# Optimization experiments

Hardware: AMD Instinct MI355X
Metric: run time of the kernel (lower is better)

## Reference

```python
import jax, jax.numpy as jnp
import numpy as np

B, D, T = 8, 512, 2048
K = 8192


def setup_inputs() -> dict:
    key = jax.random.key(0)
    k1, k2 = jax.random.split(key)
    latents = jax.random.normal(k1, (B, D, T), dtype=jnp.float32)
    # nn.Embedding weight init: uniform(-1/K, 1/K)
    embedding = jax.random.uniform(k2, (K, D), dtype=jnp.float32,
                                   minval=-1.0 / K, maxval=1.0 / K)
    return {"latents": latents, "embedding": embedding}


def reference(latents, embedding):
    # latents: [B, D, T] -> [B, T, D]
    x = jnp.transpose(latents, (0, 2, 1))
    # squared Euclidean distances (argmin identical to cdist p=2 argmin)
    x2 = jnp.sum(x * x, axis=-1, keepdims=True)          # [B, T, 1]
    e2 = jnp.sum(embedding * embedding, axis=-1)          # [K]
    xe = jnp.einsum('btd,kd->btk', x, embedding)          # [B, T, K]
    d2 = x2 - 2.0 * xe + e2                               # [B, T, K]
    ids = jnp.argmin(d2, axis=-1)                         # [B, T] int
    quantized = embedding[ids]                            # [B, T, D] gather
    return jnp.transpose(quantized, (0, 2, 1))            # [B, D, T]
```

## Files before the change

### kernel.cpp

```cpp
#include <hip/hip_runtime.h>

#define B 8
#define D 512
#define T 2048
#define K 8192
#define M (B*T)

typedef float f32x4 __attribute__((ext_vector_type(4)));
typedef short bf16x8 __attribute__((ext_vector_type(8)));
typedef unsigned short us8 __attribute__((ext_vector_type(8)));

#define CAP_SEG 48
#define WIN 1.6e-3f

#define WS_X2    0
#define WS_E2    65536
#define WS_CNT   98304
#define WS_IDS   163840
#define WS_OVFC  229376
#define WS_OVFL  229632
#define WS_BEST  295168
#define WS_GMIN  426240
#define WS_LIST  491776
#define WS_AX    6783232
#define WS_BE    23560448
#define WS_NEED  31949056

__device__ inline unsigned short f2bf(float f) {
    unsigned int x = __float_as_uint(f);
    unsigned int r = x + 0x7fffu + ((x >> 16) & 1u);
    return (unsigned short)(r >> 16);
}

__device__ inline unsigned int f2ord(float f) {
    unsigned int u = __float_as_uint(f);
    return (u & 0x80000000u) ? ~u : (u | 0x80000000u);
}
__device__ inline float ord2f(unsigned int u) {
    return __uint_as_float((u & 0x80000000u) ? (u & 0x7fffffffu) : ~u);
}

__device__ inline void gload16(const void* g, void* l) {
    __builtin_amdgcn_global_load_lds(
        (const __attribute__((address_space(1))) unsigned int*)g,
        (__attribute__((address_space(3))) unsigned int*)l, 16, 0, 0);
}

__global__ __launch_bounds__(256)
void vq_x2_init(const float* __restrict__ lat, float* __restrict__ x2g,
                unsigned int* __restrict__ cnt_seg_u32, int* __restrict__ ovfc,
                unsigned int* __restrict__ gmin) {
#pragma clang fp contract(off)
    int p = blockIdx.x * 256 + threadIdx.x;
    cnt_seg_u32[p] = 0;
    gmin[p] = 0xFFFFFFFFu;
    if (p == 0) *ovfc = 0;
    int b = p / T, t = p % T;
    const float* base = lat + (size_t)b * D * T + t;
    float blk[4];
#pragma unroll
    for (int q = 0; q < 4; q++) {
        float r[8];
#pragma unroll
        for (int j = 0; j < 8; j++) {
            float v = base[(size_t)(q * 128 + j) * T];
            r[j] = __fmul_rn(v, v);
        }
        for (int i = 8; i < 128; i += 8) {
#pragma unroll
            for (int j = 0; j < 8; j++) {
                float v = base[(size_t)(q * 128 + i + j) * T];
                r[j] = __fadd_rn(r[j], __fmul_rn(v, v));
            }
        }
        blk[q] = __fadd_rn(__fadd_rn(__fadd_rn(r[0], r[1]), __fadd_rn(r[2], r[3])),
                           __fadd_rn(__fadd_rn(r[4], r[5]), __fadd_rn(r[6], r[7])));
    }
    x2g[p] = __fadd_rn(__fadd_rn(blk[0], blk[1]), __fadd_rn(blk[2], blk[3]));
}

__global__ __launch_bounds__(256)
void vq_x2_kernel(const float* __restrict__ lat, float* __restrict__ x2g) {
#pragma clang fp contract(off)
    int p = blockIdx.x * 256 + threadIdx.x;
    int b = p / T, t = p % T;
    const float* base = lat + (size_t)b * D * T + t;
    float blk[4];
#pragma unroll
    for (int q = 0; q < 4; q++) {
        float r[8];
#pragma unroll
        for (int j = 0; j < 8; j++) {
            float v = base[(size_t)(q * 128 + j) * T];
            r[j] = __fmul_rn(v, v);
        }
        for (int i = 8; i < 128; i += 8) {
#pragma unroll
            for (int j = 0; j < 8; j++) {
                float v = base[(size_t)(q * 128 + i + j) * T];
                r[j] = __fadd_rn(r[j], __fmul_rn(v, v));
            }
        }
        blk[q] = __fadd_rn(__fadd_rn(__fadd_rn(r[0], r[1]), __fadd_rn(r[2], r[3])),
                           __fadd_rn(__fadd_rn(r[4], r[5]), __fadd_rn(r[6], r[7])));
    }
    x2g[p] = __fadd_rn(__fadd_rn(blk[0], blk[1]), __fadd_rn(blk[2], blk[3]));
}

__global__ __launch_bounds__(256)
void vq_e2_kernel(const float* __restrict__ emb, float* __restrict__ e2g) {
#pragma clang fp contract(off)
    int k = blockIdx.x * 256 + threadIdx.x;
    const float* base = emb + (size_t)k * D;
    float blk[4];
#pragma unroll
    for (int q = 0; q < 4; q++) {
        float r[8];
        {
            float4 a = *(const float4*)&base[q * 128];
            float4 c = *(const float4*)&base[q * 128 + 4];
            r[0] = __fmul_rn(a.x, a.x); r[1] = __fmul_rn(a.y, a.y);
            r[2] = __fmul_rn(a.z, a.z); r[3] = __fmul_rn(a.w, a.w);
            r[4] = __fmul_rn(c.x, c.x); r[5] = __fmul_rn(c.y, c.y);
            r[6] = __fmul_rn(c.z, c.z); r[7] = __fmul_rn(c.w, c.w);
        }
        for (int i = 8; i < 128; i += 8) {
            float4 a = *(const float4*)&base[q * 128 + i];
            float4 c = *(const float4*)&base[q * 128 + i + 4];
            r[0] = __fadd_rn(r[0], __fmul_rn(a.x, a.x));
            r[1] = __fadd_rn(r[1], __fmul_rn(a.y, a.y));
            r[2] = __fadd_rn(r[2], __fmul_rn(a.z, a.z));
            r[3] = __fadd_rn(r[3], __fmul_rn(a.w, a.w));
            r[4] = __fadd_rn(r[4], __fmul_rn(c.x, c.x));
            r[5] = __fadd_rn(r[5], __fmul_rn(c.y, c.y));
            r[6] = __fadd_rn(r[6], __fmul_rn(c.z, c.z));
            r[7] = __fadd_rn(r[7], __fmul_rn(c.w, c.w));
        }
        blk[q] = __fadd_rn(__fadd_rn(__fadd_rn(r[0], r[1]), __fadd_rn(r[2], r[3])),
                           __fadd_rn(__fadd_rn(r[4], r[5]), __fadd_rn(r[6], r[7])));
    }
    e2g[k] = __fadd_rn(__fadd_rn(blk[0], blk[1]), __fadd_rn(blk[2], blk[3]));
}

__global__ __launch_bounds__(256)
void vq_prep_a(const float* __restrict__ lat, unsigned short* __restrict__ Ax) {
    __shared__ float xsl[64][65];
    const int tid = threadIdx.x;
    const int m0 = blockIdx.x * 64;
    const int b = m0 / T, t0 = m0 % T;
    const float* lp = lat + (size_t)b * D * T + t0;
    for (int d0 = 0; d0 < D; d0 += 64) {
        if (d0) __syncthreads();
#pragma unroll
        for (int i = 0; i < 16; i++) {
            int idx = tid + i * 256;
            int dd = idx >> 6, tt = idx & 63;
            xsl[dd][tt] = lp[(size_t)(d0 + dd) * T + tt];
        }
        __syncthreads();
        int tt = tid & 63, g = tid >> 6;
        us8 va, vb;
#pragma unroll
        for (int j = 0; j < 8; j++) va[j] = f2bf(xsl[g * 16 + j][tt]);
#pragma unroll
        for (int j = 0; j < 8; j++) vb[j] = f2bf(xsl[g * 16 + 8 + j][tt]);
        *(us8*)&Ax[(size_t)(m0 + tt) * 512 + d0 + g * 16] = va;
        *(us8*)&Ax[(size_t)(m0 + tt) * 512 + d0 + g * 16 + 8] = vb;
    }
}

__global__ __launch_bounds__(256)
void vq_prep_b(const float* __restrict__ emb, unsigned short* __restrict__ Be) {
    size_t i = ((size_t)blockIdx.x * 256 + threadIdx.x) * 4;
    float4 v = *(const float4*)&emb[i];
    ushort4 o;
    o.x = f2bf(v.x); o.y = f2bf(v.y); o.z = f2bf(v.z); o.w = f2bf(v.w);
    *(ushort4*)&Be[i] = o;
}

#define BMg 128
#define BNg 128
#define NCHUNK 2048
#define NSTEPS ((NCHUNK / BNg) * 8)

__global__ __launch_bounds__(256, 2)
void vq_gemm(const unsigned short* __restrict__ Ax,
             const unsigned short* __restrict__ Be,
             const float* __restrict__ e2g,
             unsigned int* __restrict__ gmin,
             unsigned char* __restrict__ cnt_seg,
             unsigned short* __restrict__ list) {
    __shared__ unsigned short As[2][BMg * 64];
    __shared__ unsigned short Bs[2][BNg * 64];
    __shared__ float e2s[NCHUNK];
    __shared__ int cntl[BMg];

    const int tid = threadIdx.x;
    const int lane = tid & 63;
    const int wid = tid >> 6;
    const int m0 = blockIdx.x * BMg;
    const int nc0 = blockIdx.y * NCHUNK;

    for (int i = tid; i < NCHUNK; i += 256) e2s[i] = e2g[nc0 + i];
    if (tid < BMg) cntl[tid] = 0;
    asm volatile("s_waitcnt lgkmcnt(0)" ::: "memory");

    const int rbase = wid * 8 + (lane >> 3);
    const int cbyte = (((lane & 7) ^ (lane >> 3)) * 16);
    const char* gA = (const char*)Ax + (size_t)(m0 + rbase) * 1024 + cbyte;
    const char* gB = (const char*)Be + (size_t)(nc0 + rbase) * 1024 + cbyte;
    const int ldsoff = wid * 1024;

    const int rbyteA = (wid * 32 + (lane & 15)) * 128;
    const int rbyteB = ((lane & 15)) * 128;

#pragma unroll
    for (int i = 0; i < 4; i++) {
        gload16(gA + (size_t)i * 32768, (char*)As[0] + ldsoff + i * 4096);
        gload16(gB + (size_t)i * 32768, (char*)Bs[0] + ldsoff + i * 4096);
    }

    float runmin[2][4];
    float thrg[2][4];
#pragma unroll
    for (int mi = 0; mi < 2; mi++)
#pragma unroll
        for (int r = 0; r < 4; r++) runmin[mi][r] = 3.4e38f;

    f32x4 acc[2][8];
    for (int s = 0; s < NSTEPS; s++) {
        const int cur = s & 1;
        const int nt = s >> 3, ks = s & 7;

        __builtin_amdgcn_s_barrier();

        if (s + 1 < NSTEPS) {
            const int nt2 = (s + 1) >> 3, ks2 = (s + 1) & 7;
            const char* ga = gA + (size_t)(ks2 * 128);
            const char* gb = gB + (size_t)(nt2 * 128) * 1024 + (size_t)(ks2 * 128);
            char* la = (char*)As[cur ^ 1] + ldsoff;
            char* lb = (char*)Bs[cur ^ 1] + ldsoff;
#pragma unroll
            for (int i = 0; i < 4; i++) {
                gload16(ga + (size_t)i * 32768, la + i * 4096);
                gload16(gb + (size_t)i * 32768, lb + i * 4096);
            }
            asm volatile("s_waitcnt vmcnt(8)" ::: "memory");
        } else {
            asm volatile("s_waitcnt vmcnt(0)" ::: "memory");
        }
        __builtin_amdgcn_s_barrier();

        if (ks == 0) {
#pragma unroll
            for (int mi = 0; mi < 2; mi++)
#pragma unroll
                for (int ni = 0; ni < 8; ni++) acc[mi][ni] = (f32x4){0.f, 0.f, 0.f, 0.f};
#pragma unroll
            for (int mi = 0; mi < 2; mi++)
#pragma unroll
                for (int r = 0; r < 4; r++) {
                    const int m = m0 + wid * 32 + mi * 16 + (lane >> 4) * 4 + r;
                    thrg[mi][r] = ord2f(gmin[m]);
                }
        }

        __builtin_amdgcn_s_setprio(1);
#pragma unroll
        for (int kh = 0; kh < 2; kh++) {
            const int cb = ((((lane >> 4) + kh * 4) ^ (lane & 7)) * 16);
            bf16x8 af[2], bfr[8];
#pragma unroll
            for (int mi = 0; mi < 2; mi++)
                af[mi] = *(const bf16x8*)((const char*)As[cur] + rbyteA + mi * 2048 + cb);
#pragma unroll
            for (int ni = 0; ni < 8; ni++)
                bfr[ni] = *(const bf16x8*)((const char*)Bs[cur] + rbyteB + ni * 2048 + cb);
#pragma unroll
            for (int mi = 0; mi < 2; mi++)
#pragma unroll
                for (int ni = 0; ni < 8; ni++)
                    acc[mi][ni] = __builtin_amdgcn_mfma_f32_16x16x32_bf16(
                        af[mi], bfr[ni], acc[mi][ni], 0, 0, 0);
        }
        __builtin_amdgcn_s_setprio(0);

        if (ks == 7) {
            const int n0l = nt * BNg;
#pragma unroll
            for (int mi = 0; mi < 2; mi++)
#pragma unroll
                for (int ni = 0; ni < 8; ni++) {
                    float e2v = e2s[n0l + ni * 16 + (lane & 15)];
#pragma unroll
                    for (int r = 0; r < 4; r++)
                        acc[mi][ni][r] = e2v - 2.0f * acc[mi][ni][r];
                }
#pragma unroll
            for (int mi = 0; mi < 2; mi++)
#pragma unroll
                for (int r = 0; r < 4; r++) {
                    float v = acc[mi][0][r];
#pragma unroll
                    for (int ni = 1; ni < 8; ni++) v = fminf(v, acc[mi][ni][r]);
                    v = fminf(v, __shfl_xor(v, 1));
                    v = fminf(v, __shfl_xor(v, 2));
                    v = fminf(v, __shfl_xor(v, 4));
                    v = fminf(v, __shfl_xor(v, 8));
                    runmin[mi][r] = fminf(runmin[mi][r], v);
                    const int rloc = wid * 32 + mi * 16 + (lane >> 4) * 4 + r;
                    const int m = m0 + rloc;
                    float th = fminf(thrg[mi][r], runmin[mi][r]) + WIN;
#pragma unroll
                    for (int ni = 0; ni < 8; ni++) {
                        if (acc[mi][ni][r] < th) {
                            int kcode = nc0 + n0l + ni * 16 + (lane & 15);
                            int slot = atomicAdd(&cntl[rloc], 1);
                            if (slot < CAP_SEG)
                                list[m * 192 + blockIdx.y * CAP_SEG + slot] =
                                    (unsigned short)kcode;
                        }
                    }
                    if ((lane & 15) == 0)
                        atomicMin(&gmin[m], f2ord(runmin[mi][r]));
                }
        }
    }

    __syncthreads();
    if (tid < BMg) {
        int c = cntl[tid];
        cnt_seg[(size_t)(m0 + tid) * 4 + blockIdx.y] =
            (unsigned char)(c > 255 ? 255 : c);
    }
}

__global__ __launch_bounds__(256)
void vq_rescore3(const float* __restrict__ lat, const float* __restrict__ emb,
                 const float* __restrict__ x2g, const float* __restrict__ e2g,
                 const unsigned char* __restrict__ cnt_seg,
                 const unsigned short* __restrict__ list,
                 int* __restrict__ ids, int* __restrict__ ovfc,
                 int* __restrict__ ovfl, unsigned long long* __restrict__ best,
                 float* __restrict__ out) {
#pragma clang fp contract(off)
    __shared__ float xs[D][32];
    __shared__ unsigned long long bests[8][32];
    __shared__ int kid_s[32];

    const int tid = threadIdx.x;
    const int w = tid >> 5;
    const int l = tid & 31;
    const int m0 = blockIdx.x * 32;
    const int b = m0 / T, t0 = m0 % T;
    const int p = m0 + l;
    const size_t lbase = (size_t)b * D * T + t0;

#pragma unroll
    for (int i = 0; i < 64; i++) {
        int idx = tid + i * 256;
        int dd = idx >> 5, tt = idx & 31;
        xs[dd][tt] = lat[lbase + (size_t)dd * T + tt];
    }

    unsigned int cs = *(const unsigned int*)&cnt_seg[(size_t)p * 4];
    int c0 = cs & 255, c1 = (cs >> 8) & 255, c2 = (cs >> 16) & 255, c3 = (cs >> 24) & 255;
    const bool ovf = (c0 > CAP_SEG) | (c1 > CAP_SEG) | (c2 > CAP_SEG) | (c3 > CAP_SEG);
    if (w == 0 && ovf) {
        int s = atomicAdd(ovfc, 1);
        ovfl[s] = p;
        best[p] = ~0ull;
    }
    __syncthreads();

    const float x2v = x2g[p];
    unsigned long long bb = ~0ull;
    if (!ovf) {
        int segc[4] = {c0, c1, c2, c3};
#pragma unroll
        for (int seg = 0; seg < 4; seg++) {
            for (int j = w; j < segc[seg]; j += 8) {
                int k = list[(size_t)p * 192 + seg * CAP_SEG + j];
                const float4* er4 = (const float4*)(emb + (size_t)k * D);
                float acc = 0.f;
#pragma unroll 4
                for (int q = 0; q < D / 4; q++) {
                    float4 e4 = er4[q];
                    acc = __fadd_rn(acc, __fmul_rn(xs[q * 4 + 0][l], e4.x));
                    acc = __fadd_rn(acc, __fmul_rn(xs[q * 4 + 1][l], e4.y));
                    acc = __fadd_rn(acc, __fmul_rn(xs[q * 4 + 2][l], e4.z));
                    acc = __fadd_rn(acc, __fmul_rn(xs[q * 4 + 3][l], e4.w));
                }
                float tmp = __fsub_rn(x2v, __fadd_rn(acc, acc));
                float dist = __fadd_rn(tmp, e2g[k]);
                unsigned long long pk = ((unsigned long long)f2ord(dist) << 32) |
                                        (unsigned long long)(unsigned int)k;
                bb = (pk < bb) ? pk : bb;
            }
        }
    }
    bests[w][l] = bb;
    __syncthreads();

    if (tid < 32) {
        unsigned int cs2 = *(const unsigned int*)&cnt_seg[(size_t)(m0 + tid) * 4];
        bool ov2 = ((cs2 & 255) > CAP_SEG) | (((cs2 >> 8) & 255) > CAP_SEG) |
                   (((cs2 >> 16) & 255) > CAP_SEG) | (((cs2 >> 24) & 255) > CAP_SEG);
        if (!ov2) {
            unsigned long long v = bests[0][tid];
#pragma unroll
            for (int i = 1; i < 8; i++) v = (bests[i][tid] < v) ? bests[i][tid] : v;
            int kk = (int)(v & 0xFFFFFFFFull);
            ids[m0 + tid] = kk;
            kid_s[tid] = kk;
        } else {
            kid_s[tid] = -1;
        }
    }
    __syncthreads();

    float* ebuf = &xs[0][0];
    float* outb = out + (size_t)b * D * T + t0;
    for (int d0 = 0; d0 < D; d0 += 64) {
        if (d0) __syncthreads();
#pragma unroll
        for (int i = 0; i < 8; i++) {
            int idx = tid + i * 256;
            int tt = idx >> 6, dd = idx & 63;
            int kk = kid_s[tt];
            ebuf[tt * 65 + dd] = emb[(size_t)(kk < 0 ? 0 : kk) * D + d0 + dd];
        }
        __syncthreads();
#pragma unroll
        for (int i = 0; i < 8; i++) {
            int idx = tid + i * 256;
            int tt = idx & 31, dd = idx >> 5;
            if (kid_s[tt] >= 0)
                outb[(size_t)(d0 + dd) * T + tt] = ebuf[tt * 65 + dd];
        }
    }
}

__global__ __launch_bounds__(256)
void vq_fallback_par(const float* __restrict__ lat, const float* __restrict__ emb,
                     const float* __restrict__ x2g, const float* __restrict__ e2g,
                     const int* __restrict__ ovfc, const int* __restrict__ ovfl,
                     unsigned long long* __restrict__ best) {
#pragma clang fp contract(off)
    __shared__ float xr[D];
    __shared__ unsigned long long wmin[4];
    const int n = *ovfc;
    const int ntask = n * 8;
    for (int task = blockIdx.x; task < ntask; task += gridDim.x) {
        const int m = ovfl[task >> 3];
        const int slice = task & 7;
        const int b = m / T, t = m % T;
        for (int d = threadIdx.x; d < D; d += 256)
            xr[d] = lat[(size_t)b * D * T + (size_t)d * T + t];
        __syncthreads();
        const float x2v = x2g[m];
        unsigned long long bl = ~0ull;
        for (int k = slice * 1024 + threadIdx.x; k < slice * 1024 + 1024; k += 256) {
            const float* er = emb + (size_t)k * D;
            float s = 0.f;
            for (int d = 0; d < D; d++)
                s = __fadd_rn(s, __fmul_rn(xr[d], er[d]));
            float tmp = __fsub_rn(x2v, __fadd_rn(s, s));
            float dist = __fadd_rn(tmp, e2g[k]);
            unsigned long long pk = ((unsigned long long)f2ord(dist) << 32) |
                                    (unsigned long long)(unsigned int)k;
            bl = (pk < bl) ? pk : bl;
        }
#pragma unroll
        for (int off = 1; off < 64; off <<= 1) {
            unsigned long long o = __shfl_xor(bl, off);
            bl = (o < bl) ? o : bl;
        }
        if ((threadIdx.x & 63) == 0) wmin[threadIdx.x >> 6] = bl;
        __syncthreads();
        if (threadIdx.x == 0) {
            unsigned long long v = wmin[0];
            for (int i = 1; i < 4; i++) v = (wmin[i] < v) ? wmin[i] : v;
            atomicMin(&best[m], v);
        }
        __syncthreads();
    }
}

__global__ __launch_bounds__(256)
void vq_finalize(const int* __restrict__ ovfc, const int* __restrict__ ovfl,
                 const unsigned long long* __restrict__ best, int* __restrict__ ids) {
    const int n = *ovfc;
    for (int i = blockIdx.x * 256 + threadIdx.x; i < n; i += gridDim.x * 256) {
        int m = ovfl[i];
        ids[m] = (int)(best[m] & 0xFFFFFFFFull);
    }
}

__global__ __launch_bounds__(256)
void vq_gather_ovf(const float* __restrict__ emb, const int* __restrict__ ovfc,
                   const int* __restrict__ ovfl, const int* __restrict__ ids,
                   float* __restrict__ out) {
    const int n = *ovfc;
    for (int i = blockIdx.x; i < n; i += gridDim.x) {
        int m = ovfl[i];
        int b = m / T, t = m % T;
        int k = ids[m];
        for (int d = threadIdx.x; d < D; d += 256)
            out[(size_t)b * D * T + (size_t)d * T + t] = emb[(size_t)k * D + d];
    }
}

#define TM 64
#define TN 128
#define TD 32
__global__ __launch_bounds__(256)
void vq_main_old(const float* __restrict__ latents, const float* __restrict__ emb,
                 const float* __restrict__ x2g, const float* __restrict__ e2g,
                 float* __restrict__ out) {
#pragma clang fp contract(off)
    __shared__ __align__(16) float xs[TD][TM];
    __shared__ __align__(16) float es[TD][TN + 4];
    __shared__ float e2s[TN];
    __shared__ float x2s[TM];
    __shared__ int ids_s[TM];
    __shared__ __align__(16) float gbuf[64][65];
    const int tid = threadIdx.x;
    const int tn = tid & 15;
    const int tm = tid >> 4;
    const int m0 = blockIdx.x * TM;
    const int b = m0 / T;
    const int t0 = m0 % T;
    const float* lat = latents + (size_t)b * D * T + t0;
    if (tid < TM) x2s[tid] = x2g[m0 + tid];
    float minv[4];
    int mini[4];
#pragma unroll
    for (int i = 0; i < 4; i++) { minv[i] = 3.4e38f; mini[i] = 0; }
    for (int k0 = 0; k0 < K; k0 += TN) {
        __syncthreads();
        if (tid < TN) e2s[tid] = e2g[k0 + tid];
        float s[4][8];
#pragma unroll
        for (int i = 0; i < 4; i++)
#pragma unroll
            for (int j = 0; j < 8; j++) s[i][j] = 0.0f;
        for (int d0 = 0; d0 < D; d0 += TD) {
            if (d0) __syncthreads();
#pragma unroll
            for (int i = 0; i < 8; i++) {
                int idx = tid + i * 256;
                int dd = idx >> 6, tt = idx & 63;
                xs[dd][tt] = lat[(size_t)(d0 + dd) * T + tt];
            }
#pragma unroll
            for (int i = 0; i < 16; i++) {
                int idx = tid + i * 256;
                int nn = idx >> 5, dd = idx & 31;
                es[dd][nn] = emb[(size_t)(k0 + nn) * D + d0 + dd];
            }
            __syncthreads();
#pragma unroll
            for (int d = 0; d < TD; d++) {
                float4 xr = *(const float4*)&xs[d][tm * 4];
                float4 ea = *(const float4*)&es[d][tn * 4];
                float4 eb = *(const float4*)&es[d][64 + tn * 4];
                float xv[4] = {xr.x, xr.y, xr.z, xr.w};
                float ev[8] = {ea.x, ea.y, ea.z, ea.w, eb.x, eb.y, eb.z, eb.w};
#pragma unroll
                for (int i = 0; i < 4; i++)
#pragma unroll
                    for (int j = 0; j < 8; j++)
                        s[i][j] = __fadd_rn(s[i][j], __fmul_rn(xv[i], ev[j]));
            }
        }
#pragma unroll
        for (int i = 0; i < 4; i++) {
            float x2v = x2s[tm * 4 + i];
#pragma unroll
            for (int j = 0; j < 8; j++) {
                int col = (j < 4) ? (tn * 4 + j) : (64 + tn * 4 + (j - 4));
                float s2 = __fadd_rn(s[i][j], s[i][j]);
                float tmp = __fsub_rn(x2v, s2);
                float dist = __fadd_rn(tmp, e2s[col]);
                int kk = k0 + col;
                if (dist < minv[i]) { minv[i] = dist; mini[i] = kk; }
            }
        }
    }
#pragma unroll
    for (int i = 0; i < 4; i++) {
        float v1 = minv[i];
        int i1 = mini[i];
#pragma unroll
        for (int off = 1; off < 16; off <<= 1) {
            float ov = __shfl_xor(v1, off);
            int oi = __shfl_xor(i1, off);
            if (ov < v1 || (ov == v1 && oi < i1)) { v1 = ov; i1 = oi; }
        }
        if (tn == 0) ids_s[tm * 4 + i] = i1;
    }
    __syncthreads();
    float* outb = out + (size_t)b * D * T + t0;
    for (int d0 = 0; d0 < D; d0 += 64) {
        if (d0) __syncthreads();
#pragma unroll
        for (int i = 0; i < 16; i++) {
            int idx = tid + i * 256;
            int tt = idx >> 6, dd = idx & 63;
            gbuf[tt][dd] = emb[(size_t)ids_s[tt] * D + d0 + dd];
        }
        __syncthreads();
#pragma unroll
        for (int i = 0; i < 16; i++) {
            int idx = tid + i * 256;
            int dd = idx >> 6, tt = idx & 63;
            outb[(size_t)(d0 + dd) * T + tt] = gbuf[tt][dd];
        }
    }
}

extern "C" void kernel_launch(void* const* d_in, const int* in_sizes, int n_in,
                              void* d_out, int out_size, void* d_ws, size_t ws_size,
                              hipStream_t stream) {
    const float* latents = (const float*)d_in[0];
    const float* emb     = (const float*)d_in[1];
    float* out = (float*)d_out;
    char* ws = (char*)d_ws;
    float* x2g = (float*)(ws + WS_X2);
    float* e2g = (float*)(ws + WS_E2);

    if (ws_size < (size_t)WS_NEED) {
        hipLaunchKernelGGL(vq_x2_kernel, dim3(M / 256), dim3(256), 0, stream, latents, x2g);
        hipLaunchKernelGGL(vq_e2_kernel, dim3(K / 256), dim3(256), 0, stream, emb, e2g);
        hipLaunchKernelGGL(vq_main_old, dim3(M / TM), dim3(256), 0, stream,
                           latents, emb, x2g, e2g, out);
        return;
    }

    unsigned char* cnt_seg = (unsigned char*)(ws + WS_CNT);
    int* ids = (int*)(ws + WS_IDS);
    int* ovfc = (int*)(ws + WS_OVFC);
    int* ovfl = (int*)(ws + WS_OVFL);
    unsigned long long* best = (unsigned long long*)(ws + WS_BEST);
    unsigned int* gmin = (unsigned int*)(ws + WS_GMIN);
    unsigned short* list = (unsigned short*)(ws + WS_LIST);
    unsigned short* Ax = (unsigned short*)(ws + WS_AX);
    unsigned short* Be = (unsigned short*)(ws + WS_BE);

    hipLaunchKernelGGL(vq_x2_init, dim3(M / 256), dim3(256), 0, stream,
                       latents, x2g, (unsigned int*)cnt_seg, ovfc, gmin);
    hipLaunchKernelGGL(vq_e2_kernel, dim3(K / 256), dim3(256), 0, stream, emb, e2g);
    hipLaunchKernelGGL(vq_prep_a, dim3(M / 64), dim3(256), 0, stream, latents, Ax);
    hipLaunchKernelGGL(vq_prep_b, dim3((K * D) / 1024), dim3(256), 0, stream, emb, Be);
    hipLaunchKernelGGL(vq_gemm, dim3(M / BMg, K / NCHUNK), dim3(256), 0, stream,
                       Ax, Be, e2g, gmin, cnt_seg, list);
    hipLaunchKernelGGL(vq_rescore3, dim3(M / 32), dim3(256), 0, stream,
                       latents, emb, x2g, e2g, cnt_seg, list, ids, ovfc, ovfl, best, out);
    hipLaunchKernelGGL(vq_fallback_par, dim3(512), dim3(256), 0, stream,
                       latents, emb, x2g, e2g, ovfc, ovfl, best);
    hipLaunchKernelGGL(vq_finalize, dim3(64), dim3(256), 0, stream,
                       ovfc, ovfl, best, ids);
    hipLaunchKernelGGL(vq_gather_ovf, dim3(128), dim3(256), 0, stream,
                       emb, ovfc, ovfl, ids, out);
}
```

Baseline: 452.7 us.

## Single-buffer GEMM LDS for higher occupancy; unroll rescoring loop by two

The bf16 GEMM drops its double-buffered LDS tiles and the prefetch of the next K-step. Each step now loads its own tile and synchronises twice, and launch bounds rise to three blocks per CU. This trades explicit copy/compute overlap within a block for more resident blocks hiding latency. Separately, the exact fp32 rescoring loop processes two candidate codewords per iteration, sharing the shared-memory reads of x to raise memory-level parallelism.

```diff
diff --git a/kernel.cpp b/kernel.cpp
--- a/kernel.cpp
+++ b/kernel.cpp
@@ -183,15 +183,15 @@
 #define NCHUNK 2048
 #define NSTEPS ((NCHUNK / BNg) * 8)
 
-__global__ __launch_bounds__(256, 2)
+__global__ __launch_bounds__(256, 3)
 void vq_gemm(const unsigned short* __restrict__ Ax,
              const unsigned short* __restrict__ Be,
              const float* __restrict__ e2g,
              unsigned int* __restrict__ gmin,
              unsigned char* __restrict__ cnt_seg,
              unsigned short* __restrict__ list) {
-    __shared__ unsigned short As[2][BMg * 64];
-    __shared__ unsigned short Bs[2][BNg * 64];
+    __shared__ unsigned short As[BMg * 64];
+    __shared__ unsigned short Bs[BNg * 64];
     __shared__ float e2s[NCHUNK];
     __shared__ int cntl[BMg];
 
@@ -203,7 +203,6 @@
 
     for (int i = tid; i < NCHUNK; i += 256) e2s[i] = e2g[nc0 + i];
     if (tid < BMg) cntl[tid] = 0;
-    asm volatile("s_waitcnt lgkmcnt(0)" ::: "memory");
 
     const int rbase = wid * 8 + (lane >> 3);
     const int cbyte = (((lane & 7) ^ (lane >> 3)) * 16);
@@ -214,12 +213,6 @@
     const int rbyteA = (wid * 32 + (lane & 15)) * 128;
     const int rbyteB = ((lane & 15)) * 128;
 
-#pragma unroll
-    for (int i = 0; i < 4; i++) {
-        gload16(gA + (size_t)i * 32768, (char*)As[0] + ldsoff + i * 4096);
-        gload16(gB + (size_t)i * 32768, (char*)Bs[0] + ldsoff + i * 4096);
-    }
-
     float runmin[2][4];
     float thrg[2][4];
 #pragma unroll
@@ -229,27 +222,20 @@
 
     f32x4 acc[2][8];
     for (int s = 0; s < NSTEPS; s++) {
-        const int cur = s & 1;
         const int nt = s >> 3, ks = s & 7;
 
-        __builtin_amdgcn_s_barrier();
-
-        if (s + 1 < NSTEPS) {
-            const int nt2 = (s + 1) >> 3, ks2 = (s + 1) & 7;
-            const char* ga = gA + (size_t)(ks2 * 128);
-            const char* gb = gB + (size_t)(nt2 * 128) * 1024 + (size_t)(ks2 * 128);
-            char* la = (char*)As[cur ^ 1] + ldsoff;
-            char* lb = (char*)Bs[cur ^ 1] + ldsoff;
+        __syncthreads();
+
+        {
+            const char* ga = gA + (size_t)(ks * 128);
+            const char* gb = gB + (size_t)(nt * 128) * 1024 + (size_t)(ks * 128);
 #pragma unroll
             for (int i = 0; i < 4; i++) {
-                gload16(ga + (size_t)i * 32768, la + i * 4096);
-                gload16(gb + (size_t)i * 32768, lb + i * 4096);
-            }
-            asm volatile("s_waitcnt vmcnt(8)" ::: "memory");
-        } else {
-            asm volatile("s_waitcnt vmcnt(0)" ::: "memory");
-        }
-        __builtin_amdgcn_s_barrier();
+                gload16(ga + (size_t)i * 32768, (char*)As + ldsoff + i * 4096);
+                gload16(gb + (size_t)i * 32768, (char*)Bs + ldsoff + i * 4096);
+            }
+        }
+        __syncthreads();
 
         if (ks == 0) {
 #pragma unroll
@@ -272,10 +258,10 @@
             bf16x8 af[2], bfr[8];
 #pragma unroll
             for (int mi = 0; mi < 2; mi++)
-                af[mi] = *(const bf16x8*)((const char*)As[cur] + rbyteA + mi * 2048 + cb);
+                af[mi] = *(const bf16x8*)((const char*)As + rbyteA + mi * 2048 + cb);
 #pragma unroll
             for (int ni = 0; ni < 8; ni++)
-                bfr[ni] = *(const bf16x8*)((const char*)Bs[cur] + rbyteB + ni * 2048 + cb);
+                bfr[ni] = *(const bf16x8*)((const char*)Bs + rbyteB + ni * 2048 + cb);
 #pragma unroll
             for (int mi = 0; mi < 2; mi++)
 #pragma unroll
@@ -379,7 +365,39 @@
         int segc[4] = {c0, c1, c2, c3};
 #pragma unroll
         for (int seg = 0; seg < 4; seg++) {
-            for (int j = w; j < segc[seg]; j += 8) {
+            const int c = segc[seg];
+            int j = w;
+            for (; j + 8 < c; j += 16) {
+                int ka = list[(size_t)p * 192 + seg * CAP_SEG + j];
+                int kb = list[(size_t)p * 192 + seg * CAP_SEG + j + 8];
+                const float4* ea4 = (const float4*)(emb + (size_t)ka * D);
+                const float4* eb4 = (const float4*)(emb + (size_t)kb * D);
+                float aA = 0.f, aB = 0.f;
+#pragma unroll 4
+                for (int q = 0; q < D / 4; q++) {
+                    float4 va = ea4[q];
+                    float4 vb = eb4[q];
+                    float x0 = xs[q * 4 + 0][l], x1 = xs[q * 4 + 1][l];
+                    float x2_ = xs[q * 4 + 2][l], x3 = xs[q * 4 + 3][l];
+                    aA = __fadd_rn(aA, __fmul_rn(x0, va.x));
+                    aB = __fadd_rn(aB, __fmul_rn(x0, vb.x));
+                    aA = __fadd_rn(aA, __fmul_rn(x1, va.y));
+                    aB = __fadd_rn(aB, __fmul_rn(x1, vb.y));
+                    aA = __fadd_rn(aA, __fmul_rn(x2_, va.z));
+                    aB = __fadd_rn(aB, __fmul_rn(x2_, vb.z));
+                    aA = __fadd_rn(aA, __fmul_rn(x3, va.w));
+                    aB = __fadd_rn(aB, __fmul_rn(x3, vb.w));
+                }
+                float dA = __fadd_rn(__fsub_rn(x2v, __fadd_rn(aA, aA)), e2g[ka]);
+                float dB = __fadd_rn(__fsub_rn(x2v, __fadd_rn(aB, aB)), e2g[kb]);
+                unsigned long long pa = ((unsigned long long)f2ord(dA) << 32) |
+                                        (unsigned long long)(unsigned int)ka;
+                unsigned long long pb = ((unsigned long long)f2ord(dB) << 32) |
+                                        (unsigned long long)(unsigned int)kb;
+                bb = (pa < bb) ? pa : bb;
+                bb = (pb < bb) ? pb : bb;
+            }
+            if (j < c) {
                 int k = list[(size_t)p * 192 + seg * CAP_SEG + j];
                 const float4* er4 = (const float4*)(emb + (size_t)k * D);
                 float acc = 0.f;
@@ -391,8 +409,7 @@
                     acc = __fadd_rn(acc, __fmul_rn(xs[q * 4 + 2][l], e4.z));
                     acc = __fadd_rn(acc, __fmul_rn(xs[q * 4 + 3][l], e4.w));
                 }
-                float tmp = __fsub_rn(x2v, __fadd_rn(acc, acc));
-                float dist = __fadd_rn(tmp, e2g[k]);
+                float dist = __fadd_rn(__fsub_rn(x2v, __fadd_rn(acc, acc)), e2g[k]);
                 unsigned long long pk = ((unsigned long long)f2ord(dist) << 32) |
                                         (unsigned long long)(unsigned int)k;
                 bb = (pk < bb) ? pk : bb;
```

Measured after the change: 414.4 us. 1.09x faster.
